# Kernel optimization log

Measured on AMD Instinct MI355X. Metric: run time of the kernel, lower is better.

Reference implementation:

```python
import jax, jax.numpy as jnp
import numpy as np

L, B, C, OUT = 4, 4, 256, 4
H, W = 128, 128
HEADS, DH, G = 8, 32, 64
N = H * W
INNER = HEADS * DH
HID = 4 * C


def _ln(x, w, b, eps=1e-5):
    m = jnp.mean(x, -1, keepdims=True)
    v = jnp.mean((x - m) ** 2, -1, keepdims=True)
    return (x - m) / jnp.sqrt(v + eps) * w + b


def setup_inputs() -> dict:
    key = jax.random.key(0)
    ks = iter(jax.random.split(key, 16))
    nrm = lambda shape, s=0.02: jax.random.normal(next(ks), shape, jnp.float32) * s
    return dict(
        fx=jax.random.normal(next(ks), (B, N, C), jnp.float32),
        ln1_w=jnp.ones((L, C)), ln1_b=jnp.zeros((L, C)),
        convx_w=nrm((L, 3, 3, C, INNER)), convx_b=jnp.zeros((L, INNER)),
        convfx_w=nrm((L, 3, 3, C, INNER)), convfx_b=jnp.zeros((L, INNER)),
        slice_w=nrm((L, DH, G)), slice_b=jnp.zeros((L, G)),
        temperature=0.5 * jnp.ones((L, HEADS)),
        wq=nrm((L, DH, DH)), wk=nrm((L, DH, DH)), wv=nrm((L, DH, DH)),
        wo=nrm((L, INNER, C)), bo=jnp.zeros((L, C)),
        ln2_w=jnp.ones((L, C)), ln2_b=jnp.zeros((L, C)),
        w1=nrm((L, C, HID)), b1=jnp.zeros((L, HID)),
        w2=nrm((L, HID, C)), b2=jnp.zeros((L, C)),
        ln3_w=jnp.ones((C,)), ln3_b=jnp.zeros((C,)),
        w_out=nrm((C, OUT)), b_out=jnp.zeros((OUT,)),
    )


def reference(fx, ln1_w, ln1_b, convx_w, convx_b, convfx_w, convfx_b,
              slice_w, slice_b, temperature, wq, wk, wv, wo, bo,
              ln2_w, ln2_b, w1, b1, w2, b2, ln3_w, ln3_b, w_out, b_out):
    Bb = fx.shape[0]
    scale = DH ** -0.5
    for i in range(L):
        # --- Physics attention (slice attention) ---
        x = _ln(fx, ln1_w[i], ln1_b[i])
        ximg = x.reshape(Bb, H, W, C)  # NHWC
        conv = lambda w, b: jax.lax.conv_general_dilated(
            ximg, w, (1, 1), 'SAME',
            dimension_numbers=('NHWC', 'HWIO', 'NHWC')) + b
        fx_mid = conv(convfx_w[i], convfx_b[i]).reshape(Bb, N, HEADS, DH).transpose(0, 2, 1, 3)  # [B,h,N,d]
        x_mid = conv(convx_w[i], convx_b[i]).reshape(Bb, N, HEADS, DH).transpose(0, 2, 1, 3)
        temp = jnp.clip(temperature[i], 0.1, 5.0)[None, :, None, None]
        logits = (jnp.einsum('bhnd,dg->bhng', x_mid, slice_w[i]) + slice_b[i]) / temp
        sw = jax.nn.softmax(logits, axis=-1)  # [B,h,N,G]
        norm = sw.sum(2)  # [B,h,G]
        st = jnp.einsum('bhnc,bhng->bhgc', fx_mid, sw) / (norm + 1e-5)[..., None]  # [B,h,G,d]
        q = jnp.einsum('bhgc,cd->bhgd', st, wq[i])
        k = jnp.einsum('bhgc,cd->bhgd', st, wk[i])
        v = jnp.einsum('bhgc,cd->bhgd', st, wv[i])
        attn = jax.nn.softmax(jnp.einsum('bhgd,bhkd->bhgk', q, k) * scale, axis=-1)
        ot = jnp.einsum('bhgk,bhkd->bhgd', attn, v)  # [B,h,G,d]
        out_x = jnp.einsum('bhgc,bhng->bhnc', ot, sw)  # deslice back to points
        out_x = out_x.transpose(0, 2, 1, 3).reshape(Bb, N, INNER)
        fx = fx + out_x @ wo[i] + bo[i]
        # --- MLP (n_layers=0, no res inside) ---
        h = _ln(fx, ln2_w[i], ln2_b[i])
        h = jax.nn.gelu(h @ w1[i] + b1[i], approximate=False) @ w2[i] + b2[i]
        fx = fx + h
    # last-layer head
    return _ln(fx, ln3_w, ln3_b) @ w_out + b_out
```

## Files before the change

kernel.cpp:

```cpp
#include <hip/hip_runtime.h>
#include <hip/hip_bf16.h>

typedef __hip_bfloat16 bf16;
typedef __bf16 bfv8 __attribute__((ext_vector_type(8)));
typedef float f32x4 __attribute__((ext_vector_type(4)));

#define BB 4
#define HH 128
#define WWI 128
#define NN 16384
#define CC 256
#define LL 4
#define NHEADS 8
#define DHD 32
#define GG 64
#define INNERC 256
#define HIDD 1024
#define SPLIT 32
#define SSP 16

__device__ __forceinline__ float b2f(bf16 x) { return __bfloat162float(x); }
__device__ __forceinline__ bf16 f2b(float x) { return __float2bfloat16(x); }
__device__ __forceinline__ float us2f(unsigned short v) {
  return __uint_as_float(((unsigned)v) << 16);
}
__device__ __forceinline__ unsigned short b2us(bf16 h) {
  union { bf16 b; unsigned short u; } c; c.b = h; return c.u;
}

__device__ __forceinline__ void async16(void* l, const void* g) {
  __builtin_amdgcn_global_load_lds(
      (const __attribute__((address_space(1))) void*)g,
      (__attribute__((address_space(3))) void*)l, 16, 0, 0);
}

__device__ __forceinline__ float wave_sum(float v) {
#pragma unroll
  for (int off = 32; off > 0; off >>= 1) v += __shfl_down(v, off, 64);
  return v;
}

__device__ __forceinline__ float gelu_exact(float x) {
  return 0.5f * x * (1.0f + erff(x * 0.70710678118654752f));
}

__global__ void transpose_cast_kernel(const float* __restrict__ src, bf16* __restrict__ dst,
                                      int R, int Cm) {
  __shared__ float tile[32][33];
  int tb = blockIdx.z;
  const float* s = src + (size_t)tb * R * Cm;
  bf16* d = dst + (size_t)tb * R * Cm;
  int c0 = blockIdx.x * 32, r0 = blockIdx.y * 32;
  int tx = threadIdx.x & 31, ty = threadIdx.x >> 5;
  for (int rr = ty; rr < 32; rr += 8) {
    int r = r0 + rr, c = c0 + tx;
    tile[rr][tx] = (r < R && c < Cm) ? s[(size_t)r * Cm + c] : 0.f;
  }
  __syncthreads();
  for (int cc = ty; cc < 32; cc += 8) {
    int c = c0 + cc, r = r0 + tx;
    if (c < Cm && r < R) d[(size_t)c * R + r] = f2b(tile[tx][cc]);
  }
}

__global__ __launch_bounds__(256) void ln_kernel(const float* __restrict__ x,
                                                 const float* __restrict__ w,
                                                 const float* __restrict__ b,
                                                 bf16* __restrict__ out) {
  int wid = threadIdx.x >> 6, lane = threadIdx.x & 63;
  int p = blockIdx.x * 4 + wid;
  float4 v = ((const float4*)(x + (size_t)p * CC))[lane];
  float s = v.x + v.y + v.z + v.w;
  float sq = v.x * v.x + v.y * v.y + v.z * v.z + v.w * v.w;
#pragma unroll
  for (int off = 32; off > 0; off >>= 1) {
    s += __shfl_xor(s, off, 64);
    sq += __shfl_xor(sq, off, 64);
  }
  float mean = s * (1.0f / CC);
  float var = sq * (1.0f / CC) - mean * mean;
  float rstd = rsqrtf(var + 1e-5f);
  float4 wv = ((const float4*)w)[lane];
  float4 bv = ((const float4*)b)[lane];
  unsigned short o0 = b2us(f2b((v.x - mean) * rstd * wv.x + bv.x));
  unsigned short o1 = b2us(f2b((v.y - mean) * rstd * wv.y + bv.y));
  unsigned short o2 = b2us(f2b((v.z - mean) * rstd * wv.z + bv.z));
  unsigned short o3 = b2us(f2b((v.w - mean) * rstd * wv.w + bv.w));
  uint2 pk = make_uint2((unsigned)o0 | ((unsigned)o1 << 16),
                        (unsigned)o2 | ((unsigned)o3 << 16));
  ((uint2*)(out + (size_t)p * CC))[lane] = pk;
}

__global__ __launch_bounds__(512) void conv_mfma_kernel(
    const bf16* __restrict__ xln, const bf16* __restrict__ wt,
    const float* __restrict__ bias, bf16* __restrict__ out,
    const float* __restrict__ zbuf) {
  __shared__ __align__(16) unsigned short As[3 * 130 * 64];
  __shared__ __align__(16) unsigned short Bsm[2][256 * 64];
  int bid = blockIdx.x;
  bid = (bid & 7) * 64 + (bid >> 3);
  int h = bid & 127;
  int b = bid >> 7;
  int t = threadIdx.x, lane = t & 63, wid = t >> 6;
  int wm = (wid & 1) * 64, wn = (wid >> 1) * 64;
  int l15 = lane & 15, l4 = lane >> 4;
  int wu = t & ~63;
  f32x4 acc[4][4];
#pragma unroll
  for (int mi = 0; mi < 4; ++mi)
#pragma unroll
    for (int ni = 0; ni < 4; ++ni) acc[mi][ni] = (f32x4){0.f, 0.f, 0.f, 0.f};
  const bf16* xbase = xln + (size_t)b * NN * CC;

  for (int q = 0; q < 4; ++q) {
#pragma unroll
    for (int k = 0; k < 6; ++k) {
      int u = t + k * 512;
      int jp = u & 7, pc = u >> 3;
      int r = pc / 130, cl = pc - r * 130;
      int j = jp ^ (cl & 7);
      int gr = h + r - 1, gc = cl - 1;
      const void* src =
          ((unsigned)gr < 128u && (unsigned)gc < 128u)
              ? (const void*)(xbase + ((size_t)(gr * WWI + gc)) * CC + q * 64 + j * 8)
              : (const void*)zbuf;
      async16(&As[(size_t)(wu + k * 512) * 8], src);
    }
    if (t < 48) {
      int u = t + 3072;
      int jp = u & 7, pc = u >> 3;
      int r = pc / 130, cl = pc - r * 130;
      int j = jp ^ (cl & 7);
      int gr = h + r - 1, gc = cl - 1;
      uint4 v = make_uint4(0u, 0u, 0u, 0u);
      if ((unsigned)gr < 128u && (unsigned)gc < 128u)
        v = *(const uint4*)(xbase + ((size_t)(gr * WWI + gc)) * CC + q * 64 + j * 8);
      *(uint4*)(&As[(size_t)u * 8]) = v;
    }
#pragma unroll
    for (int k = 0; k < 4; ++k) {
      int u = t + k * 512;
      int n = u >> 3, jp = u & 7, j = jp ^ (n & 7);
      async16(&Bsm[0][(size_t)(wu + k * 512) * 8],
              wt + (size_t)n * 256 + q * 64 + j * 8);
    }
    __syncthreads();

    for (int tap = 0; tap < 9; ++tap) {
      int cur = tap & 1;
      if (tap < 8) {
#pragma unroll
        for (int k = 0; k < 4; ++k) {
          int u = t + k * 512;
          int n = u >> 3, jp = u & 7, j = jp ^ (n & 7);
          async16(&Bsm[cur ^ 1][(size_t)(wu + k * 512) * 8],
                  wt + ((size_t)((tap + 1) * 256 + n)) * 256 + q * 64 + j * 8);
        }
      }
      int ky = tap / 3, kx = tap - ky * 3;
      const unsigned short* Bc = Bsm[cur];
#pragma unroll
      for (int s = 0; s < 2; ++s) {
        bfv8 af[4], bfr[4];
#pragma unroll
        for (int mi = 0; mi < 4; ++mi) {
          int cl = wm + mi * 16 + l15 + kx;
          af[mi] = *(const bfv8*)(&As[((size_t)(ky * 130 + cl)) * 64 +
                                      (((s * 4 + l4) ^ (cl & 7)) << 3)]);
        }
#pragma unroll
        for (int ni = 0; ni < 4; ++ni) {
          int rn = wn + ni * 16 + l15;
          bfr[ni] = *(const bfv8*)(&Bc[(size_t)rn * 64 + (((s * 4 + l4) ^ (rn & 7)) << 3)]);
        }
#pragma unroll
        for (int mi = 0; mi < 4; ++mi)
#pragma unroll
          for (int ni = 0; ni < 4; ++ni)
            acc[mi][ni] = __builtin_amdgcn_mfma_f32_16x16x32_bf16(af[mi], bfr[ni], acc[mi][ni], 0, 0, 0);
      }
      __syncthreads();
    }
  }
  int colB = wn + l15;
  int rowB = wm + l4 * 4;
#pragma unroll
  for (int ni = 0; ni < 4; ++ni) {
    int oc = colB + ni * 16;
    float bv = bias[oc];
#pragma unroll
    for (int mi = 0; mi < 4; ++mi) {
#pragma unroll
      for (int r = 0; r < 4; ++r) {
        int pix = rowB + mi * 16 + r;
        out[((size_t)(b * NN + h * WWI + pix)) * CC + oc] = f2b(acc[mi][ni][r] + bv);
      }
    }
  }
}

__global__ __launch_bounds__(256, 2) void gemm_acc_kernel(
    const bf16* __restrict__ A, const bf16* __restrict__ BT,
    const float* __restrict__ bias, float* __restrict__ outf,
    int M, int N, int K, size_t strideAz, size_t strideBz, size_t strideOz) {
  A  += (size_t)blockIdx.z * strideAz;
  BT += (size_t)blockIdx.z * strideBz;
  __shared__ __align__(16) unsigned short As[128 * 64];
  __shared__ __align__(16) unsigned short Bs[128 * 64];
  int m0 = blockIdx.x * 128, n0 = blockIdx.y * 128;
  int t = threadIdx.x, lane = t & 63, wid = t >> 6;
  int wm = (wid >> 1) * 64, wn = (wid & 1) * 64;
  int l15 = lane & 15, q4 = lane >> 4;
  int wg = wm >> 4, ng = wn >> 4;
  f32x4 acc[4][4];
#pragma unroll
  for (int mi = 0; mi < 4; ++mi)
#pragma unroll
    for (int ni = 0; ni < 4; ++ni) acc[mi][ni] = (f32x4){0.f, 0.f, 0.f, 0.f};

  for (int kb = 0; kb < K; kb += 64) {
    __syncthreads();
#pragma unroll
    for (int i = 0; i < 4; ++i) {
      int inst = wid * 4 + i;
      int g = inst >> 1, h2 = inst & 1;
      int row = g * 16 + l15;
      int kc = (h2 * 4 + q4) * 8;
      async16(&As[(size_t)g * 1024 + h2 * 512], A + (size_t)(m0 + row) * K + kb + kc);
      async16(&Bs[(size_t)g * 1024 + h2 * 512], BT + (size_t)(n0 + row) * K + kb + kc);
    }
    __syncthreads();
#pragma unroll
    for (int s = 0; s < 2; ++s) {
      int kgrp = s * 4 + q4;
      bfv8 af[4], bfr[4];
#pragma unroll
      for (int mi = 0; mi < 4; ++mi)
        af[mi] = *(const bfv8*)(&As[(size_t)(wg + mi) * 1024 + kgrp * 128 + l15 * 8]);
#pragma unroll
      for (int ni = 0; ni < 4; ++ni)
        bfr[ni] = *(const bfv8*)(&Bs[(size_t)(ng + ni) * 1024 + kgrp * 128 + l15 * 8]);
#pragma unroll
      for (int mi = 0; mi < 4; ++mi)
#pragma unroll
        for (int ni = 0; ni < 4; ++ni)
          acc[mi][ni] = __builtin_amdgcn_mfma_f32_16x16x32_bf16(af[mi], bfr[ni], acc[mi][ni], 0, 0, 0);
    }
  }
  int colB = n0 + wn + l15;
  int rowB = m0 + wm + q4 * 4;
#pragma unroll
  for (int ni = 0; ni < 4; ++ni) {
    int col = colB + ni * 16;
    float bv = bias[col];
#pragma unroll
    for (int mi = 0; mi < 4; ++mi) {
#pragma unroll
      for (int r = 0; r < 4; ++r) {
        int row = rowB + mi * 16 + r;
        outf[(size_t)blockIdx.z * strideOz + (size_t)row * N + col] += acc[mi][ni][r] + bv;
      }
    }
  }
}

__global__ __launch_bounds__(512, 4) void mlp_fused_kernel(
    const bf16* __restrict__ xln, const bf16* __restrict__ w1t,
    const float* __restrict__ b1, const bf16* __restrict__ w2t,
    const float* __restrict__ b2, float* __restrict__ fx) {
  __shared__ __align__(16) unsigned short As[64 * 256];
  __shared__ __align__(16) bf16 Hs[64 * 128];
  __shared__ __align__(16) unsigned short Wb[256 * 64];
  int m0 = blockIdx.x * 64;
  int t = threadIdx.x, lane = t & 63, wid = t >> 6;
  int l15 = lane & 15, q4 = lane >> 4;
  int wm2 = (wid & 1) * 32, wn2 = (wid >> 1) * 32;
  int wm = (wid & 1) * 32, wn = (wid >> 1) * 64;

  const unsigned short* xg = (const unsigned short*)xln + (size_t)m0 * 256;
#pragma unroll
  for (int i = 0; i < 4; ++i) {
    int u = t + i * 512;
    int row = u >> 5, v = u & 31;
    int kb = v >> 3, jp = v & 7;
    uint4 val = ((const uint4*)xg)[u];
    ((uint4*)As)[row * 32 + kb * 8 + (jp ^ (row & 7))] = val;
  }

  f32x4 accO[2][4];
#pragma unroll
  for (int mi = 0; mi < 2; ++mi)
#pragma unroll
    for (int ni = 0; ni < 4; ++ni) accO[mi][ni] = (f32x4){0.f, 0.f, 0.f, 0.f};

  for (int j = 0; j < 8; ++j) {
    int hbase = j * 128;
    f32x4 acc2[2][2];
#pragma unroll
    for (int mi = 0; mi < 2; ++mi)
#pragma unroll
      for (int nj = 0; nj < 2; ++nj) acc2[mi][nj] = (f32x4){0.f, 0.f, 0.f, 0.f};
    for (int kb = 0; kb < 4; ++kb) {
      __syncthreads();
#pragma unroll
      for (int i = 0; i < 2; ++i) {
        int u = t + i * 512;
        int n = u >> 3, jp = u & 7;
        uint4 val = *(const uint4*)(w1t + (size_t)(hbase + n) * 256 + kb * 64 + jp * 8);
        ((uint4*)Wb)[n * 8 + (jp ^ (n & 7))] = val;
      }
      __syncthreads();
#pragma unroll
      for (int ks = 0; ks < 2; ++ks) {
        int kgrp = ks * 4 + q4;
        bfv8 af[2], bfr[2];
#pragma unroll
        for (int mi = 0; mi < 2; ++mi) {
          int row = wm2 + mi * 16 + l15;
          af[mi] = *(const bfv8*)(&As[row * 256 + kb * 64 + ((kgrp ^ (row & 7)) << 3)]);
        }
#pragma unroll
        for (int nj = 0; nj < 2; ++nj) {
          int n = wn2 + nj * 16 + l15;
          bfr[nj] = *(const bfv8*)(&Wb[n * 64 + ((kgrp ^ (n & 7)) << 3)]);
        }
#pragma unroll
        for (int mi = 0; mi < 2; ++mi)
#pragma unroll
          for (int nj = 0; nj < 2; ++nj)
            acc2[mi][nj] = __builtin_amdgcn_mfma_f32_16x16x32_bf16(af[mi], bfr[nj], acc2[mi][nj], 0, 0, 0);
      }
    }
#pragma unroll
    for (int nj = 0; nj < 2; ++nj) {
      int coln = wn2 + nj * 16 + l15;
      float bv = b1[hbase + coln];
      int half = coln >> 6, sub = (coln >> 3) & 7, lo = coln & 7;
#pragma unroll
      for (int mi = 0; mi < 2; ++mi) {
#pragma unroll
        for (int r = 0; r < 4; ++r) {
          int row = wm2 + mi * 16 + q4 * 4 + r;
          float v = acc2[mi][nj][r] + bv;
          Hs[row * 128 + half * 64 + (((sub ^ (row & 7)) << 3) + lo)] = f2b(gelu_exact(v));
        }
      }
    }
    for (int kb2 = 0; kb2 < 2; ++kb2) {
      __syncthreads();
#pragma unroll
      for (int i = 0; i < 4; ++i) {
        int u = t + i * 512;
        int n = u >> 3, jp = u & 7;
        uint4 val = *(const uint4*)(w2t + (size_t)n * 1024 + hbase + kb2 * 64 + jp * 8);
        ((uint4*)Wb)[n * 8 + (jp ^ (n & 7))] = val;
      }
      __syncthreads();
#pragma unroll
      for (int ks = 0; ks < 2; ++ks) {
        int kgrp = ks * 4 + q4;
        bfv8 af[2], bfr[4];
#pragma unroll
        for (int mi = 0; mi < 2; ++mi) {
          int row = wm + mi * 16 + l15;
          af[mi] = *(const bfv8*)(&Hs[row * 128 + kb2 * 64 + ((kgrp ^ (row & 7)) << 3)]);
        }
#pragma unroll
        for (int ni = 0; ni < 4; ++ni) {
          int n = wn + ni * 16 + l15;
          bfr[ni] = *(const bfv8*)(&Wb[n * 64 + ((kgrp ^ (n & 7)) << 3)]);
        }
#pragma unroll
        for (int mi = 0; mi < 2; ++mi)
#pragma unroll
          for (int ni = 0; ni < 4; ++ni)
            accO[mi][ni] = __builtin_amdgcn_mfma_f32_16x16x32_bf16(af[mi], bfr[ni], accO[mi][ni], 0, 0, 0);
      }
    }
  }
#pragma unroll
  for (int ni = 0; ni < 4; ++ni) {
    int col = wn + ni * 16 + l15;
    float bv = b2[col];
#pragma unroll
    for (int mi = 0; mi < 2; ++mi) {
#pragma unroll
      for (int r = 0; r < 4; ++r) {
        int row = m0 + wm + mi * 16 + q4 * 4 + r;
        fx[(size_t)row * 256 + col] += accO[mi][ni][r] + bv;
      }
    }
  }
}

__global__ __launch_bounds__(256) void slice_softmax_kernel(
    const bf16* __restrict__ xmid, const float* __restrict__ sw_w,
    const float* __restrict__ sw_b, const float* __restrict__ temp,
    bf16* __restrict__ swout) {
  __shared__ float wsm[32][64];
  __shared__ float xm[SSP][256];
  __shared__ float bias_s[64];
  __shared__ float rtc[8];
  int p0 = blockIdx.x * SSP;
  int t = threadIdx.x;
  for (int i = t; i < 2048; i += 256) wsm[i >> 6][i & 63] = sw_w[i];
  if (t < 64) bias_s[t] = sw_b[t];
  if (t < 8) {
    float x = temp[t];
    rtc[t] = 1.0f / fminf(fmaxf(x, 0.1f), 5.0f);
  }
  const unsigned short* xg = (const unsigned short*)xmid + (size_t)p0 * 256;
#pragma unroll
  for (int i2 = t; i2 < SSP * 32; i2 += 256) {
    uint4 v = ((const uint4*)xg)[i2];
    int p = i2 >> 5, c = (i2 & 31) << 3;
    xm[p][c + 0] = us2f((unsigned short)(v.x & 0xffff));
    xm[p][c + 1] = us2f((unsigned short)(v.x >> 16));
    xm[p][c + 2] = us2f((unsigned short)(v.y & 0xffff));
    xm[p][c + 3] = us2f((unsigned short)(v.y >> 16));
    xm[p][c + 4] = us2f((unsigned short)(v.z & 0xffff));
    xm[p][c + 5] = us2f((unsigned short)(v.z >> 16));
    xm[p][c + 6] = us2f((unsigned short)(v.w & 0xffff));
    xm[p][c + 7] = us2f((unsigned short)(v.w >> 16));
  }
  __syncthreads();
  int g = t & 63, pq = t >> 6;
  for (int pp2 = 0; pp2 < SSP / 4; ++pp2) {
    int p = pp2 * 4 + pq;
#pragma unroll
    for (int h = 0; h < NHEADS; ++h) {
      float acc = bias_s[g];
      const float* xr = &xm[p][h * 32];
#pragma unroll
      for (int d = 0; d < 32; ++d) acc += xr[d] * wsm[d][g];
      float logit = acc * rtc[h];
      float m = logit;
#pragma unroll
      for (int off = 32; off > 0; off >>= 1) m = fmaxf(m, __shfl_xor(m, off, 64));
      float e = __expf(logit - m);
      float s = e;
#pragma unroll
      for (int off = 32; off > 0; off >>= 1) s += __shfl_xor(s, off, 64);
      swout[(size_t)(p0 + p) * 512 + h * 64 + g] = f2b(e / s);
    }
  }
}

__global__ __launch_bounds__(256) void slice_st_kernel(
    const bf16* __restrict__ fxmid, const bf16* __restrict__ sw,
    float* __restrict__ stp, float* __restrict__ normp) {
  __shared__ __align__(16) unsigned short sw_s[64 * 64];
  __shared__ __align__(16) unsigned short fx_s[32 * 64];
  __shared__ float npart[2][64];
  int split = blockIdx.x, h = blockIdx.y, b = blockIdx.z;
  int t = threadIdx.x, w = t >> 6, lane = t & 63;
  int l15 = lane & 15, q4 = lane >> 4;
  int ns0 = split * (NN / SPLIT);
  const int NT = (NN / SPLIT) / 64;
  f32x4 acc0 = {0.f, 0.f, 0.f, 0.f}, acc1 = {0.f, 0.f, 0.f, 0.f};
  float nacc = 0.f;
  const unsigned short* swg = (const unsigned short*)sw + (size_t)b * NN * 512 + h * 64;
  const unsigned short* fxg = (const unsigned short*)fxmid + (size_t)b * NN * 256 + h * 32;

  for (int kt = 0; kt < NT; ++kt) {
    int n0 = ns0 + kt * 64;
    __syncthreads();
    if (w < 2) {
      int g = lane;
#pragma unroll
      for (int i = 0; i < 4; ++i) {
        int j = w + 2 * i;
        const unsigned short* p = swg + (size_t)(n0 + j * 8) * 512 + g;
        unsigned short v0 = p[0],     v1 = p[512],  v2 = p[1024], v3 = p[1536];
        unsigned short v4 = p[2048],  v5 = p[2560], v6 = p[3072], v7 = p[3584];
        nacc += us2f(v0) + us2f(v1) + us2f(v2) + us2f(v3) +
                us2f(v4) + us2f(v5) + us2f(v6) + us2f(v7);
        uint4 pk = make_uint4((unsigned)v0 | ((unsigned)v1 << 16),
                              (unsigned)v2 | ((unsigned)v3 << 16),
                              (unsigned)v4 | ((unsigned)v5 << 16),
                              (unsigned)v6 | ((unsigned)v7 << 16));
        ((uint4*)sw_s)[g * 8 + (j ^ (g & 7))] = pk;
      }
    } else {
      int d = lane & 31, nh = lane >> 5, w3 = w - 2;
#pragma unroll
      for (int i = 0; i < 2; ++i) {
        int nbase = (w3 * 2 + i) * 16 + nh * 8;
        const unsigned short* p = fxg + (size_t)(n0 + nbase) * 256 + d;
        unsigned short v0 = p[0],    v1 = p[256],  v2 = p[512],  v3 = p[768];
        unsigned short v4 = p[1024], v5 = p[1280], v6 = p[1536], v7 = p[1792];
        uint4 pk = make_uint4((unsigned)v0 | ((unsigned)v1 << 16),
                              (unsigned)v2 | ((unsigned)v3 << 16),
                              (unsigned)v4 | ((unsigned)v5 << 16),
                              (unsigned)v6 | ((unsigned)v7 << 16));
        int u = nbase >> 3;
        ((uint4*)fx_s)[d * 8 + (u ^ (d & 7))] = pk;
      }
    }
    __syncthreads();
    int gg = w * 16 + l15;
    int d0 = l15, d1 = 16 + l15;
#pragma unroll
    for (int ks = 0; ks < 2; ++ks) {
      bfv8 af  = ((const bfv8*)sw_s)[gg * 8 + ((ks * 4 + q4) ^ (gg & 7))];
      bfv8 bf0 = ((const bfv8*)fx_s)[d0 * 8 + ((ks * 4 + q4) ^ (d0 & 7))];
      bfv8 bf1 = ((const bfv8*)fx_s)[d1 * 8 + ((ks * 4 + q4) ^ (d1 & 7))];
      acc0 = __builtin_amdgcn_mfma_f32_16x16x32_bf16(af, bf0, acc0, 0, 0, 0);
      acc1 = __builtin_amdgcn_mfma_f32_16x16x32_bf16(af, bf1, acc1, 0, 0, 0);
    }
  }
  if (w < 2) npart[w][lane] = nacc;
  __syncthreads();
  int bh = b * NHEADS + h;
  if (t < 64) normp[(size_t)split * (BB * NHEADS * GG) + bh * 64 + t] = npart[0][t] + npart[1][t];
  size_t base = ((size_t)split * (BB * NHEADS * GG) + bh * 64) * 32;
#pragma unroll
  for (int r = 0; r < 4; ++r) {
    int g = w * 16 + q4 * 4 + r;
    stp[base + (size_t)g * 32 + l15] = acc0[r];
    stp[base + (size_t)g * 32 + 16 + l15] = acc1[r];
  }
}

__global__ __launch_bounds__(256) void attn_kernel(
    const float* __restrict__ stp, const float* __restrict__ normp,
    const float* __restrict__ wq, const float* __restrict__ wk,
    const float* __restrict__ wv, float* __restrict__ ot) {
  __shared__ float wqs[32 * 32], wks[32 * 32], wvs[32 * 32];
  __shared__ float st[GG][DHD + 1];
  __shared__ float qq[GG][DHD + 1], kk[GG][DHD + 1], vv[GG][DHD + 1];
  __shared__ float pm[GG][GG + 1];
  __shared__ float nrm[GG];
  int bh = blockIdx.x;
  int t = threadIdx.x;
  ((float4*)wqs)[t] = ((const float4*)wq)[t];
  ((float4*)wks)[t] = ((const float4*)wk)[t];
  ((float4*)wvs)[t] = ((const float4*)wv)[t];
  if (t < 64) {
    float ns = 0.f;
    for (int s = 0; s < SPLIT; ++s) ns += normp[(size_t)s * (BB * NHEADS * GG) + bh * 64 + t];
    nrm[t] = 1.0f / (ns + 1e-5f);
  }
  __syncthreads();
#pragma unroll
  for (int i = 0; i < 8; ++i) {
    int idx = t + i * 256;
    int g = idx >> 5, d = idx & 31;
    float a = 0.f;
    for (int s = 0; s < SPLIT; ++s)
      a += stp[((size_t)s * (BB * NHEADS * GG) + bh * 64 + g) * 32 + d];
    st[g][d] = a * nrm[g];
  }
  __syncthreads();
#pragma unroll
  for (int i = 0; i < 8; ++i) {
    int idx = t + i * 256;
    int g = idx >> 5, d = idx & 31;
    float aq = 0.f, ak = 0.f, av = 0.f;
#pragma unroll
    for (int c = 0; c < 32; ++c) {
      float sv = st[g][c];
      aq += sv * wqs[c * 32 + d];
      ak += sv * wks[c * 32 + d];
      av += sv * wvs[c * 32 + d];
    }
    qq[g][d] = aq; kk[g][d] = ak; vv[g][d] = av;
  }
  __syncthreads();
  {
    int g = t >> 2, sub = t & 3;
    float sc[16];
    float m = -1e30f;
    const float scale = 0.17677669529663687f;
#pragma unroll
    for (int jj = 0; jj < 16; ++jj) {
      int j = sub * 16 + jj;
      float a = 0.f;
#pragma unroll
      for (int d = 0; d < 32; ++d) a += qq[g][d] * kk[j][d];
      a *= scale;
      sc[jj] = a;
      m = fmaxf(m, a);
    }
    m = fmaxf(m, __shfl_xor(m, 1, 64));
    m = fmaxf(m, __shfl_xor(m, 2, 64));
    float ssum = 0.f;
#pragma unroll
    for (int jj = 0; jj < 16; ++jj) { sc[jj] = __expf(sc[jj] - m); ssum += sc[jj]; }
    ssum += __shfl_xor(ssum, 1, 64);
    ssum += __shfl_xor(ssum, 2, 64);
    float rs = 1.0f / ssum;
#pragma unroll
    for (int jj = 0; jj < 16; ++jj) pm[g][sub * 16 + jj] = sc[jj] * rs;
  }
  __syncthreads();
#pragma unroll
  for (int i = 0; i < 8; ++i) {
    int idx = t + i * 256;
    int g = idx >> 5, d = idx & 31;
    float a = 0.f;
#pragma unroll
    for (int j = 0; j < GG; ++j) a += pm[g][j] * vv[j][d];
    ot[((size_t)bh * GG + g) * DHD + d] = a;
  }
}

__global__ __launch_bounds__(256) void wc_kernel(const float* __restrict__ ot,
                                                 const float* __restrict__ wo,
                                                 bf16* __restrict__ wct) {
  __shared__ float ots[GG][DHD];
  int bh = blockIdx.x;
  int h = bh & 7, b = bh >> 3;
  int t = threadIdx.x;
  for (int i = t; i < GG * DHD; i += 256) ots[i >> 5][i & 31] = ot[(size_t)bh * (GG * DHD) + i];
  float wol[DHD];
#pragma unroll
  for (int d = 0; d < DHD; ++d) wol[d] = wo[(size_t)(h * DHD + d) * CC + t];
  __syncthreads();
  bf16* dst = wct + ((size_t)b * CC + t) * (NHEADS * GG) + h * GG;
#pragma unroll 4
  for (int g = 0; g < GG; ++g) {
    float a = 0.f;
#pragma unroll
    for (int d = 0; d < DHD; ++d) a += wol[d] * ots[g][d];
    dst[g] = f2b(a);
  }
}

__global__ __launch_bounds__(256) void head_kernel(const float* __restrict__ fx,
                                                   const float* __restrict__ w,
                                                   const float* __restrict__ b,
                                                   const float* __restrict__ wout,
                                                   const float* __restrict__ bout,
                                                   float* __restrict__ out) {
  int wid = threadIdx.x >> 6, lane = threadIdx.x & 63;
  int p = blockIdx.x * 4 + wid;
  float4 v = ((const float4*)(fx + (size_t)p * CC))[lane];
  float s = v.x + v.y + v.z + v.w;
  float sq = v.x * v.x + v.y * v.y + v.z * v.z + v.w * v.w;
#pragma unroll
  for (int off = 32; off > 0; off >>= 1) {
    s += __shfl_xor(s, off, 64);
    sq += __shfl_xor(sq, off, 64);
  }
  float mean = s * (1.0f / CC);
  float var = sq * (1.0f / CC) - mean * mean;
  float rstd = rsqrtf(var + 1e-5f);
  float4 wv = ((const float4*)w)[lane];
  float4 bv = ((const float4*)b)[lane];
  float xn0 = (v.x - mean) * rstd * wv.x + bv.x;
  float xn1 = (v.y - mean) * rstd * wv.y + bv.y;
  float xn2 = (v.z - mean) * rstd * wv.z + bv.z;
  float xn3 = (v.w - mean) * rstd * wv.w + bv.w;
  float4 w0 = ((const float4*)wout)[lane * 4 + 0];
  float4 w1 = ((const float4*)wout)[lane * 4 + 1];
  float4 w2 = ((const float4*)wout)[lane * 4 + 2];
  float4 w3 = ((const float4*)wout)[lane * 4 + 3];
  float4 o;
  o.x = xn0 * w0.x + xn1 * w1.x + xn2 * w2.x + xn3 * w3.x;
  o.y = xn0 * w0.y + xn1 * w1.y + xn2 * w2.y + xn3 * w3.y;
  o.z = xn0 * w0.z + xn1 * w1.z + xn2 * w2.z + xn3 * w3.z;
  o.w = xn0 * w0.w + xn1 * w1.w + xn2 * w2.w + xn3 * w3.w;
#pragma unroll
  for (int off = 32; off > 0; off >>= 1) {
    o.x += __shfl_xor(o.x, off, 64);
    o.y += __shfl_xor(o.y, off, 64);
    o.z += __shfl_xor(o.z, off, 64);
    o.w += __shfl_xor(o.w, off, 64);
  }
  if (lane == 0) {
    float4 bo4 = *((const float4*)bout);
    float4 r;
    r.x = o.x + bo4.x; r.y = o.y + bo4.y; r.z = o.z + bo4.z; r.w = o.w + bo4.w;
    ((float4*)out)[p] = r;
  }
}

extern "C" void kernel_launch(void* const* d_in, const int* in_sizes, int n_in,
                              void* d_out, int out_size, void* d_ws, size_t ws_size,
                              hipStream_t stream) {
  const float* fx_in      = (const float*)d_in[0];
  const float* ln1_w      = (const float*)d_in[1];
  const float* ln1_b      = (const float*)d_in[2];
  const float* convx_w    = (const float*)d_in[3];
  const float* convx_b    = (const float*)d_in[4];
  const float* convfx_w   = (const float*)d_in[5];
  const float* convfx_b   = (const float*)d_in[6];
  const float* slice_w    = (const float*)d_in[7];
  const float* slice_b    = (const float*)d_in[8];
  const float* temperature= (const float*)d_in[9];
  const float* wq         = (const float*)d_in[10];
  const float* wk         = (const float*)d_in[11];
  const float* wv         = (const float*)d_in[12];
  const float* wo         = (const float*)d_in[13];
  const float* bo         = (const float*)d_in[14];
  const float* ln2_w      = (const float*)d_in[15];
  const float* ln2_b      = (const float*)d_in[16];
  const float* w1         = (const float*)d_in[17];
  const float* b1         = (const float*)d_in[18];
  const float* w2         = (const float*)d_in[19];
  const float* b2         = (const float*)d_in[20];
  const float* ln3_w      = (const float*)d_in[21];
  const float* ln3_b      = (const float*)d_in[22];
  const float* w_out      = (const float*)d_in[23];
  const float* b_out      = (const float*)d_in[24];
  float* out = (float*)d_out;

  char* ws = (char*)d_ws;
  size_t off = 0;
  auto alloc = [&](size_t bytes) -> void* {
    void* p = ws + off;
    off += (bytes + 255) & ~(size_t)255;
    return p;
  };
  float* fx32  = (float*)alloc((size_t)BB * NN * CC * 4);
  bf16* xln    = (bf16*)alloc((size_t)BB * NN * CC * 2);
  char* uni    = (char*)alloc((size_t)BB * NN * 512 * 2 * 2);
  bf16* xmid   = (bf16*)uni;
  bf16* fxmid  = (bf16*)(uni + (size_t)BB * NN * INNERC * 2);
  bf16* swb    = (bf16*)(uni + (size_t)2 * BB * NN * INNERC * 2);
  float* stp   = (float*)uni;
  float* normp = (float*)(uni + (size_t)SPLIT * BB * NHEADS * GG * DHD * 4);
  bf16* wtx    = (bf16*)alloc((size_t)LL * 9 * CC * INNERC * 2);
  bf16* wtfx   = (bf16*)alloc((size_t)LL * 9 * CC * INNERC * 2);
  bf16* w1t    = (bf16*)alloc((size_t)LL * CC * HIDD * 2);
  bf16* w2t    = (bf16*)alloc((size_t)LL * HIDD * CC * 2);
  float* otb   = (float*)alloc((size_t)BB * NHEADS * GG * DHD * 4);
  bf16* wct    = (bf16*)alloc((size_t)BB * CC * NHEADS * GG * 2);
  float* zbuf  = (float*)alloc(256);
  (void)ws_size; (void)in_sizes; (void)n_in; (void)out_size;

  hipMemsetAsync(zbuf, 0, 256, stream);

  transpose_cast_kernel<<<dim3(8, 8, LL * 9), 256, 0, stream>>>(convx_w, wtx, CC, INNERC);
  transpose_cast_kernel<<<dim3(8, 8, LL * 9), 256, 0, stream>>>(convfx_w, wtfx, CC, INNERC);
  transpose_cast_kernel<<<dim3(32, 8, LL), 256, 0, stream>>>(w1, w1t, CC, HIDD);
  transpose_cast_kernel<<<dim3(8, 32, LL), 256, 0, stream>>>(w2, w2t, HIDD, CC);

  hipMemcpyAsync(fx32, fx_in, (size_t)BB * NN * CC * sizeof(float),
                 hipMemcpyDeviceToDevice, stream);

  const int M = BB * NN;
  for (int i = 0; i < LL; ++i) {
    ln_kernel<<<M / 4, 256, 0, stream>>>(fx32, ln1_w + i * CC, ln1_b + i * CC, xln);
    conv_mfma_kernel<<<BB * HH, 512, 0, stream>>>(
        xln, wtfx + (size_t)i * 9 * CC * INNERC, convfx_b + i * INNERC, fxmid,
        (const float*)zbuf);
    conv_mfma_kernel<<<BB * HH, 512, 0, stream>>>(
        xln, wtx + (size_t)i * 9 * CC * INNERC, convx_b + i * INNERC, xmid,
        (const float*)zbuf);
    slice_softmax_kernel<<<M / SSP, 256, 0, stream>>>(
        xmid, slice_w + i * DHD * GG, slice_b + i * GG, temperature + i * NHEADS, swb);
    slice_st_kernel<<<dim3(SPLIT, NHEADS, BB), 256, 0, stream>>>(fxmid, swb, stp, normp);
    attn_kernel<<<BB * NHEADS, 256, 0, stream>>>(
        stp, normp, wq + i * DHD * DHD, wk + i * DHD * DHD, wv + i * DHD * DHD, otb);
    wc_kernel<<<BB * NHEADS, 256, 0, stream>>>(otb, wo + (size_t)i * INNERC * CC, wct);
    gemm_acc_kernel<<<dim3(NN / 128, CC / 128, BB), 256, 0, stream>>>(
        swb, wct, bo + i * CC, fx32, NN, CC, NHEADS * GG,
        (size_t)NN * (NHEADS * GG), (size_t)CC * (NHEADS * GG), (size_t)NN * CC);
    ln_kernel<<<M / 4, 256, 0, stream>>>(fx32, ln2_w + i * CC, ln2_b + i * CC, xln);
    mlp_fused_kernel<<<M / 64, 512, 0, stream>>>(
        xln, w1t + (size_t)i * CC * HIDD, b1 + i * HIDD,
        w2t + (size_t)i * HIDD * CC, b2 + i * CC, fx32);
  }
  head_kernel<<<M / 4, 256, 0, stream>>>(fx32, ln3_w, ln3_b, w_out, b_out, out);
}
```

Before: 2.337 ms.

## Compute two output rows per conv block to reuse weight tiles

Each conv block now computes two image rows instead of one. It stages a 4-row input halo and doubles the per-wave M tile to 8 MFMA fragments, so every staged weight tile feeds twice as many outputs and the halo overhead per output drops. The weight prefetch also continues across channel-quarter boundaries, and the scalar tail load becomes an async copy. The grid is halved, and register pressure and LDS use (about 132KB) rise, which limits each CU to one block.

```diff
diff --git a/kernel.cpp b/kernel.cpp
--- a/kernel.cpp
+++ b/kernel.cpp
@@ -91,81 +91,80 @@
   ((uint2*)(out + (size_t)p * CC))[lane] = pk;
 }
 
-__global__ __launch_bounds__(512) void conv_mfma_kernel(
+__global__ __launch_bounds__(512, 2) void conv_mfma_kernel(
     const bf16* __restrict__ xln, const bf16* __restrict__ wt,
     const float* __restrict__ bias, bf16* __restrict__ out,
     const float* __restrict__ zbuf) {
-  __shared__ __align__(16) unsigned short As[3 * 130 * 64];
+  __shared__ __align__(16) unsigned short As[4 * 130 * 64];
   __shared__ __align__(16) unsigned short Bsm[2][256 * 64];
   int bid = blockIdx.x;
-  bid = (bid & 7) * 64 + (bid >> 3);
-  int h = bid & 127;
-  int b = bid >> 7;
+  bid = (bid & 7) * 32 + (bid >> 3);
+  int h0 = (bid & 63) * 2;
+  int b = bid >> 6;
   int t = threadIdx.x, lane = t & 63, wid = t >> 6;
-  int wm = (wid & 1) * 64, wn = (wid >> 1) * 64;
+  int r = wid & 1;
+  int wn = (wid >> 1) * 64;
   int l15 = lane & 15, l4 = lane >> 4;
   int wu = t & ~63;
-  f32x4 acc[4][4];
-#pragma unroll
-  for (int mi = 0; mi < 4; ++mi)
+  f32x4 acc[8][4];
+#pragma unroll
+  for (int mi = 0; mi < 8; ++mi)
 #pragma unroll
     for (int ni = 0; ni < 4; ++ni) acc[mi][ni] = (f32x4){0.f, 0.f, 0.f, 0.f};
   const bf16* xbase = xln + (size_t)b * NN * CC;
 
+  auto stageB = [&](int buf, int tap, int q) {
+#pragma unroll
+    for (int k = 0; k < 4; ++k) {
+      int u = t + k * 512;
+      int n = u >> 3, jp = u & 7, j = jp ^ (n & 7);
+      async16(&Bsm[buf][(size_t)(wu + k * 512) * 8],
+              wt + ((size_t)(tap * 256 + n)) * 256 + q * 64 + j * 8);
+    }
+  };
+
   for (int q = 0; q < 4; ++q) {
 #pragma unroll
-    for (int k = 0; k < 6; ++k) {
+    for (int k = 0; k < 8; ++k) {
       int u = t + k * 512;
       int jp = u & 7, pc = u >> 3;
-      int r = pc / 130, cl = pc - r * 130;
+      int ar = pc / 130, cl = pc - ar * 130;
       int j = jp ^ (cl & 7);
-      int gr = h + r - 1, gc = cl - 1;
+      int gr = h0 + ar - 1, gc = cl - 1;
       const void* src =
           ((unsigned)gr < 128u && (unsigned)gc < 128u)
               ? (const void*)(xbase + ((size_t)(gr * WWI + gc)) * CC + q * 64 + j * 8)
               : (const void*)zbuf;
       async16(&As[(size_t)(wu + k * 512) * 8], src);
     }
-    if (t < 48) {
-      int u = t + 3072;
+    if (t < 64) {
+      int u = t + 4096;
       int jp = u & 7, pc = u >> 3;
-      int r = pc / 130, cl = pc - r * 130;
+      int ar = pc / 130, cl = pc - ar * 130;
       int j = jp ^ (cl & 7);
-      int gr = h + r - 1, gc = cl - 1;
-      uint4 v = make_uint4(0u, 0u, 0u, 0u);
-      if ((unsigned)gr < 128u && (unsigned)gc < 128u)
-        v = *(const uint4*)(xbase + ((size_t)(gr * WWI + gc)) * CC + q * 64 + j * 8);
-      *(uint4*)(&As[(size_t)u * 8]) = v;
-    }
-#pragma unroll
-    for (int k = 0; k < 4; ++k) {
-      int u = t + k * 512;
-      int n = u >> 3, jp = u & 7, j = jp ^ (n & 7);
-      async16(&Bsm[0][(size_t)(wu + k * 512) * 8],
-              wt + (size_t)n * 256 + q * 64 + j * 8);
-    }
+      int gr = h0 + ar - 1, gc = cl - 1;
+      const void* src =
+          ((unsigned)gr < 128u && (unsigned)gc < 128u)
+              ? (const void*)(xbase + ((size_t)(gr * WWI + gc)) * CC + q * 64 + j * 8)
+              : (const void*)zbuf;
+      async16(&As[(size_t)4096 * 8], src);
+    }
+    if (q == 0) stageB(0, 0, 0);
     __syncthreads();
 
     for (int tap = 0; tap < 9; ++tap) {
-      int cur = tap & 1;
-      if (tap < 8) {
-#pragma unroll
-        for (int k = 0; k < 4; ++k) {
-          int u = t + k * 512;
-          int n = u >> 3, jp = u & 7, j = jp ^ (n & 7);
-          async16(&Bsm[cur ^ 1][(size_t)(wu + k * 512) * 8],
-                  wt + ((size_t)((tap + 1) * 256 + n)) * 256 + q * 64 + j * 8);
-        }
-      }
+      int cur = (q * 9 + tap) & 1;
+      if (tap < 8)      stageB(cur ^ 1, tap + 1, q);
+      else if (q < 3)   stageB(cur ^ 1, 0, q + 1);
       int ky = tap / 3, kx = tap - ky * 3;
       const unsigned short* Bc = Bsm[cur];
 #pragma unroll
       for (int s = 0; s < 2; ++s) {
-        bfv8 af[4], bfr[4];
-#pragma unroll
-        for (int mi = 0; mi < 4; ++mi) {
-          int cl = wm + mi * 16 + l15 + kx;
-          af[mi] = *(const bfv8*)(&As[((size_t)(ky * 130 + cl)) * 64 +
+        bfv8 af[8], bfr[4];
+#pragma unroll
+        for (int mi = 0; mi < 8; ++mi) {
+          int cl = mi * 16 + l15 + kx;
+          af[mi] = *(const bfv8*)(&As[((size_t)((ky + r) * 130 + cl)) * 64 +
                                       (((s * 4 + l4) ^ (cl & 7)) << 3)]);
         }
 #pragma unroll
@@ -174,7 +173,7 @@
           bfr[ni] = *(const bfv8*)(&Bc[(size_t)rn * 64 + (((s * 4 + l4) ^ (rn & 7)) << 3)]);
         }
 #pragma unroll
-        for (int mi = 0; mi < 4; ++mi)
+        for (int mi = 0; mi < 8; ++mi)
 #pragma unroll
           for (int ni = 0; ni < 4; ++ni)
             acc[mi][ni] = __builtin_amdgcn_mfma_f32_16x16x32_bf16(af[mi], bfr[ni], acc[mi][ni], 0, 0, 0);
@@ -183,17 +182,17 @@
     }
   }
   int colB = wn + l15;
-  int rowB = wm + l4 * 4;
+  int rowB = l4 * 4;
 #pragma unroll
   for (int ni = 0; ni < 4; ++ni) {
     int oc = colB + ni * 16;
     float bv = bias[oc];
 #pragma unroll
-    for (int mi = 0; mi < 4; ++mi) {
-#pragma unroll
-      for (int r = 0; r < 4; ++r) {
-        int pix = rowB + mi * 16 + r;
-        out[((size_t)(b * NN + h * WWI + pix)) * CC + oc] = f2b(acc[mi][ni][r] + bv);
+    for (int mi = 0; mi < 8; ++mi) {
+#pragma unroll
+      for (int rr = 0; rr < 4; ++rr) {
+        int pix = mi * 16 + rowB + rr;
+        out[((size_t)(b * NN + (h0 + r) * WWI + pix)) * CC + oc] = f2b(acc[mi][ni][rr] + bv);
       }
     }
   }
@@ -743,10 +742,10 @@
   const int M = BB * NN;
   for (int i = 0; i < LL; ++i) {
     ln_kernel<<<M / 4, 256, 0, stream>>>(fx32, ln1_w + i * CC, ln1_b + i * CC, xln);
-    conv_mfma_kernel<<<BB * HH, 512, 0, stream>>>(
+    conv_mfma_kernel<<<BB * HH / 2, 512, 0, stream>>>(
         xln, wtfx + (size_t)i * 9 * CC * INNERC, convfx_b + i * INNERC, fxmid,
         (const float*)zbuf);
-    conv_mfma_kernel<<<BB * HH, 512, 0, stream>>>(
+    conv_mfma_kernel<<<BB * HH / 2, 512, 0, stream>>>(
         xln, wtx + (size_t)i * 9 * CC * INNERC, convx_b + i * INNERC, xmid,
         (const float*)zbuf);
     slice_softmax_kernel<<<M / SSP, 256, 0, stream>>>(
```

Measured after the change: 2.296 ms. No clear change (-1.7%).
